# Optimization experiments

Hardware: AMD Instinct MI355X
Metric: run time of the kernel (lower is better)

## Reference

```python
import jax, jax.numpy as jnp
import numpy as np

N = 100000      # nodes
D = 64          # input feature dim
L0, L1 = 64, 32 # layer sizes
EP = 400000     # positive edges
EN = 400000     # negative edges
LAMB = 1.0


def _scatter_mean(feats, rows, num_nodes):
    # mean of feats grouped by destination node `rows`; empty nodes -> 0
    s = jax.ops.segment_sum(feats, rows, num_segments=num_nodes)
    c = jax.ops.segment_sum(jnp.ones((rows.shape[0],), feats.dtype), rows, num_segments=num_nodes)
    return s / jnp.maximum(c, 1.0)[:, None]


def _base_layer(x, edges, W, b):
    row, col = edges[0], edges[1]
    agg = _scatter_mean(x[col], row, x.shape[0])          # [N, D]
    return jnp.tanh(jnp.concatenate([agg, x], axis=1) @ W + b)


def _deep_layer(x1, x2, pos_edges, neg_edges, W, b):
    agg1 = _scatter_mean(x1[pos_edges[1]], pos_edges[0], x1.shape[0])
    agg2 = _scatter_mean(x2[neg_edges[1]], neg_edges[0], x2.shape[0])
    return jnp.tanh(jnp.concatenate([agg1, agg2, x1], axis=1) @ W + b)


def _xavier(key, shape):
    fan_in, fan_out = shape[0], shape[1]
    lim = np.sqrt(6.0 / (fan_in + fan_out)).astype(np.float32)
    return jax.random.uniform(key, shape, jnp.float32, -lim, lim)


def setup_inputs() -> dict:
    key = jax.random.key(0)
    ks = jax.random.split(key, 12)
    X = jax.random.normal(ks[0], (N, D), jnp.float32)
    W_pos0 = _xavier(ks[1], (2 * D, L0)); b_pos0 = jnp.zeros((L0,), jnp.float32)
    W_neg0 = _xavier(ks[2], (2 * D, L0)); b_neg0 = jnp.zeros((L0,), jnp.float32)
    W_pos1 = _xavier(ks[3], (3 * L0, L1)); b_pos1 = jnp.zeros((L1,), jnp.float32)
    W_neg1 = _xavier(ks[4], (3 * L0, L1)); b_neg1 = jnp.zeros((L1,), jnp.float32)
    W_reg = _xavier(ks[5], (4 * L1, 2))
    positive_edges = jax.random.randint(ks[6], (2, EP), 0, N)
    negative_edges = jax.random.randint(ks[7], (2, EN), 0, N)
    target = jax.random.randint(ks[8], (EP + EN,), 0, 2)
    pos_samples = jax.random.randint(ks[9], (EP,), 0, N)
    neg_samples = jax.random.randint(ks[10], (EN,), 0, N)
    return {"X": X, "W_pos0": W_pos0, "b_pos0": b_pos0, "W_neg0": W_neg0,
            "b_neg0": b_neg0, "W_pos1": W_pos1, "b_pos1": b_pos1,
            "W_neg1": W_neg1, "b_neg1": b_neg1, "W_reg": W_reg,
            "positive_edges": positive_edges, "negative_edges": negative_edges,
            "target": target, "pos_samples": pos_samples, "neg_samples": neg_samples}


def _triplet_loss(z, edges, samples):
    zi = z[edges[0]]
    zj = z[edges[1]]
    zk = z[samples]
    norm_ij = jnp.sum((zi - zj) ** 2, axis=1)
    norm_ik = jnp.sum((zj - zk) ** 2, axis=1)
    return jnp.mean(jnp.maximum(norm_ij - norm_ik, 0.0)), zi, zj


def reference(X, W_pos0, b_pos0, W_neg0, b_neg0, W_pos1, b_pos1,
              W_neg1, b_neg1, W_reg, positive_edges, negative_edges,
              target, pos_samples, neg_samples):
    h_pos = _base_layer(X, positive_edges, W_pos0, b_pos0)
    h_neg = _base_layer(X, negative_edges, W_neg0, b_neg0)
    h_pos2 = _deep_layer(h_pos, h_neg, positive_edges, negative_edges, W_pos1, b_pos1)
    h_neg2 = _deep_layer(h_neg, h_pos, positive_edges, negative_edges, W_neg1, b_neg1)
    z = jnp.concatenate([h_pos2, h_neg2], axis=1)  # [N, 2*L1]

    loss_pos, pzi, pzj = _triplet_loss(z, positive_edges, pos_samples)
    loss_neg, nzi, nzj = _triplet_loss(z, negative_edges, neg_samples)

    feats = jnp.concatenate([
        jnp.concatenate([pzi, pzj], axis=1),
        jnp.concatenate([nzi, nzj], axis=1)], axis=0)       # [EP+EN, 4*L1]
    logp = jax.nn.log_softmax(feats @ W_reg, axis=1)
    regress = -jnp.mean(jnp.take_along_axis(logp, target[:, None], axis=1))
    loss = regress + LAMB * (loss_pos + loss_neg)
    return (loss, z)
```

## Files before the change

kernel.cpp:

```cpp
#include <hip/hip_runtime.h>
#include <cstdint>

#define N_NODES 100000
#define EP_N 400000
#define EN_N 400000
#define NODE_BLOCKS ((N_NODES + 63) / 64)
#define DEEP_BLOCKS (N_NODES / 32)
#define SCHUNK 512
#define SBLK ((N_NODES + SCHUNK - 1) / SCHUNK)

#define BSTR 264
#define DSTR 392

#define XB_BLKS ((((N_NODES + 1) * 16) + 255) / 256)
#define WP_BLKS 112
#define CNT_BLKS (((EP_N + EN_N) + 255) / 256)
#define EI_BLKS CNT_BLKS

#define ACC_OFF 0
#define I_CNTP 16
#define I_CNTN (I_CNTP + N_NODES)
#define I_CURP (I_CNTN + N_NODES)
#define I_CURN (I_CURP + N_NODES)
#define I_OFFP (I_CURN + N_NODES)
#define I_OFFN (I_OFFP + N_NODES + 1)
#define I_CSRP (((I_OFFN + N_NODES + 1) + 3) & ~3)
#define CSR_SZ (EP_N + 4 * N_NODES)
#define I_CSRN (I_CSRP + CSR_SZ)
#define I_PART (I_CSRN + CSR_SZ)
#define I_EIDX (((I_PART + 2 * SBLK) + 3) & ~3)
#define F_XB (((I_EIDX + 4 * (EP_N + EN_N)) + 15) & ~15)
#define F_HB (F_XB + 32 * (N_NODES + 1))
#define F_HQ (F_HB + 64 * (N_NODES + 1))
#define F_PNU (F_HQ + 32 * (N_NODES + 1))
#define F_PNV (F_PNU + 4 * N_NODES)
#define F_ZQ (F_PNV + 4 * N_NODES)
#define F_WT (((F_ZQ + 16 * N_NODES) + 15) & ~15)

typedef __attribute__((ext_vector_type(8))) short sh8;
typedef __attribute__((ext_vector_type(4))) float f32x4;

__device__ inline float bf2f(unsigned short u) {
    return __uint_as_float((unsigned)u << 16);
}
__device__ inline unsigned short f2bf(float v) {
    unsigned u = __float_as_uint(v);
    return (unsigned short)((u + 0x7FFFu + ((u >> 16) & 1u)) >> 16);
}
__device__ inline float lo_bf(unsigned u) { return __uint_as_float(u << 16); }
__device__ inline float hi_bf(unsigned u) { return __uint_as_float(u & 0xFFFF0000u); }

__device__ inline float dot4f8(unsigned a, unsigned b) {
    float s = __builtin_amdgcn_cvt_f32_fp8(a, 0) * __builtin_amdgcn_cvt_f32_fp8(b, 0);
    s = fmaf(__builtin_amdgcn_cvt_f32_fp8(a, 1), __builtin_amdgcn_cvt_f32_fp8(b, 1), s);
    s = fmaf(__builtin_amdgcn_cvt_f32_fp8(a, 2), __builtin_amdgcn_cvt_f32_fp8(b, 2), s);
    s = fmaf(__builtin_amdgcn_cvt_f32_fp8(a, 3), __builtin_amdgcn_cvt_f32_fp8(b, 3), s);
    return s;
}

__global__ void prep_kernel(const float* __restrict__ X, unsigned short* __restrict__ xb,
                            const float* __restrict__ W0p, const float* __restrict__ W0n,
                            const float* __restrict__ W1p, const float* __restrict__ W1n,
                            unsigned short* __restrict__ wt,
                            const int* __restrict__ pe, const int* __restrict__ ne,
                            const int* __restrict__ ps, const int* __restrict__ ns,
                            const int* __restrict__ tgt,
                            int* cp, int* cn, int4* __restrict__ eidx) {
    int b = blockIdx.x;
    if (b < XB_BLKS) {
        int i = b * 256 + threadIdx.x;
        if (i < (N_NODES + 1) * 16) {
            ushort4 o = {0, 0, 0, 0};
            if (i < N_NODES * 16) {
                float4 v = ((const float4*)X)[i];
                o.x = f2bf(v.x); o.y = f2bf(v.y); o.z = f2bf(v.z); o.w = f2bf(v.w);
            }
            ((ushort4*)xb)[i] = o;
        }
    } else if (b < XB_BLKS + WP_BLKS) {
        int i = (b - XB_BLKS) * 256 + threadIdx.x;
        if (i < 8192) {
            int n = i >> 7, k = i & 127;
            wt[i] = f2bf(W0p[k * 64 + n]);
        } else if (i < 16384) {
            int j = i - 8192; int n = j >> 7, k = j & 127;
            wt[i] = f2bf(W0n[k * 64 + n]);
        } else if (i < 22528) {
            int j = i - 16384; int n = j / 192, k = j - n * 192;
            wt[i] = f2bf(W1p[k * 32 + n]);
        } else if (i < 28672) {
            int j = i - 22528; int n = j / 192, k = j - n * 192;
            wt[i] = f2bf(W1n[k * 32 + n]);
        }
    } else if (b < XB_BLKS + WP_BLKS + CNT_BLKS) {
        int i = (b - XB_BLKS - WP_BLKS) * 256 + threadIdx.x;
        if (i < EP_N) {
            atomicAdd(&cp[pe[i]], 1);
        } else if (i < EP_N + EN_N) {
            atomicAdd(&cn[ne[i - EP_N]], 1);
        }
    } else {
        int e = (b - XB_BLKS - WP_BLKS - CNT_BLKS) * 256 + threadIdx.x;
        if (e < EP_N) {
            int4 q = {pe[e], pe[EP_N + e], ps[e], tgt[e]};
            eidx[e] = q;
        } else if (e < EP_N + EN_N) {
            int e2 = e - EP_N;
            int4 q = {ne[e2], ne[EN_N + e2], ns[e2], tgt[e]};
            eidx[e] = q;
        }
    }
}

__global__ __launch_bounds__(512) void scan_p1(const int* __restrict__ cntP,
                                               const int* __restrict__ cntN,
                                               int* part) {
    int l = blockIdx.x < SBLK ? 0 : 1;
    int blk = blockIdx.x - l * SBLK;
    const int* cnt = l == 0 ? cntP : cntN;
    int idx = blk * SCHUNK + threadIdx.x;
    int v = idx < N_NODES ? (cnt[idx] + 3) & ~3 : 0;
    __shared__ int tmp[512];
    tmp[threadIdx.x] = v;
    __syncthreads();
    for (int d = 256; d > 0; d >>= 1) {
        if (threadIdx.x < d) tmp[threadIdx.x] += tmp[threadIdx.x + d];
        __syncthreads();
    }
    if (threadIdx.x == 0) part[l * SBLK + blk] = tmp[0];
}

__global__ __launch_bounds__(512) void scan_p2(int* part) {
    int t = threadIdx.x;
    int l = t >> 8, idx = t & 255;
    int v = idx < SBLK ? part[l * SBLK + idx] : 0;
    __shared__ int tmp[512];
    int sb = l << 8;
    tmp[sb + idx] = v;
    __syncthreads();
    for (int d = 1; d < 256; d <<= 1) {
        int x = (idx >= d) ? tmp[sb + idx - d] : 0;
        __syncthreads();
        tmp[sb + idx] += x;
        __syncthreads();
    }
    if (idx < SBLK) part[l * SBLK + idx] = tmp[sb + idx] - v;
}

__global__ __launch_bounds__(512) void scan_p3(const int* __restrict__ cntP,
                                               const int* __restrict__ cntN,
                                               const int* __restrict__ part,
                                               int* offP, int* offN,
                                               int* csrP, int* csrN) {
    int l = blockIdx.x < SBLK ? 0 : 1;
    int blk = blockIdx.x - l * SBLK;
    const int* cnt = l == 0 ? cntP : cntN;
    int* off = l == 0 ? offP : offN;
    int* csr = l == 0 ? csrP : csrN;
    int base = part[l * SBLK + blk];
    int t = threadIdx.x;
    int gidx = blk * SCHUNK + t;
    int c = gidx < N_NODES ? cnt[gidx] : 0;
    int cpad = (c + 3) & ~3;
    __shared__ int tmp[512];
    tmp[t] = cpad;
    __syncthreads();
    for (int d = 1; d < 512; d <<= 1) {
        int x = (t >= d) ? tmp[t - d] : 0;
        __syncthreads();
        tmp[t] += x;
        __syncthreads();
    }
    int incl = tmp[t];
    if (gidx < N_NODES) {
        int o = base + incl - cpad;
        off[gidx] = o;
        for (int p = c; p < cpad; ++p) csr[o + p] = N_NODES;
    }
    if (gidx == N_NODES - 1) off[N_NODES] = base + incl;
}

__global__ void fill_kernel(const int* __restrict__ pe, const int* __restrict__ ne,
                            const int* __restrict__ offP, const int* __restrict__ offN,
                            int* curP, int* curN, int* csrP, int* csrN) {
    int e = blockIdx.x * 256 + threadIdx.x;
    if (e < EP_N) {
        int row = pe[e], col = pe[EP_N + e];
        int slot = atomicAdd(&curP[row], 1);
        csrP[offP[row] + slot] = col;
    } else if (e < EP_N + EN_N) {
        int e2 = e - EP_N;
        int row = ne[e2], col = ne[EN_N + e2];
        int slot = atomicAdd(&curN[row], 1);
        csrN[offN[row] + slot] = col;
    }
}

__device__ inline void gmb2w(const unsigned* __restrict__ xb32,
                             const int* __restrict__ csrP, int pP, int enP, int cP,
                             const int* __restrict__ csrN, int pN, int enN, int cN,
                             int hf, int l5,
                             float& gP0, float& gP1, float& gN0, float& gN1) {
    float a0 = 0.f, a1 = 0.f, b0 = 0.f, b1 = 0.f;
    while (pP < enP && pN < enN) {
        int4 ca = *(const int4*)(csrP + pP);
        int4 cb = *(const int4*)(csrN + pN);
        int cA0 = hf ? ca.y : ca.x;
        int cA1 = hf ? ca.w : ca.z;
        int cB0 = hf ? cb.y : cb.x;
        int cB1 = hf ? cb.w : cb.z;
        unsigned va0 = xb32[cA0 * 32 + l5];
        unsigned va1 = xb32[cA1 * 32 + l5];
        unsigned vb0 = xb32[cB0 * 32 + l5];
        unsigned vb1 = xb32[cB1 * 32 + l5];
        a0 += lo_bf(va0) + lo_bf(va1);
        a1 += hi_bf(va0) + hi_bf(va1);
        b0 += lo_bf(vb0) + lo_bf(vb1);
        b1 += hi_bf(vb0) + hi_bf(vb1);
        pP += 4; pN += 4;
    }
    for (; pP < enP; pP += 4) {
        int4 ca = *(const int4*)(csrP + pP);
        int cA0 = hf ? ca.y : ca.x;
        int cA1 = hf ? ca.w : ca.z;
        unsigned va0 = xb32[cA0 * 32 + l5];
        unsigned va1 = xb32[cA1 * 32 + l5];
        a0 += lo_bf(va0) + lo_bf(va1);
        a1 += hi_bf(va0) + hi_bf(va1);
    }
    for (; pN < enN; pN += 4) {
        int4 cb = *(const int4*)(csrN + pN);
        int cB0 = hf ? cb.y : cb.x;
        int cB1 = hf ? cb.w : cb.z;
        unsigned vb0 = xb32[cB0 * 32 + l5];
        unsigned vb1 = xb32[cB1 * 32 + l5];
        b0 += lo_bf(vb0) + lo_bf(vb1);
        b1 += hi_bf(vb0) + hi_bf(vb1);
    }
    a0 += __shfl_xor(a0, 32); a1 += __shfl_xor(a1, 32);
    b0 += __shfl_xor(b0, 32); b1 += __shfl_xor(b1, 32);
    float rP = 1.f / fmaxf((float)cP, 1.f), rN = 1.f / fmaxf((float)cN, 1.f);
    gP0 = a0 * rP; gP1 = a1 * rP;
    gN0 = b0 * rN; gN1 = b1 * rN;
}

__device__ inline void gd2q(const unsigned* __restrict__ hq32,
                            const int* __restrict__ csrP, int pP, int enP, int cP,
                            const int* __restrict__ csrN, int pN, int enN, int cN,
                            int hf, int l5,
                            float& gPp0, float& gPp1, float& gPn0, float& gPn1,
                            float& gNp0, float& gNp1, float& gNn0, float& gNn1) {
    float ap0 = 0.f, ap1 = 0.f, an0 = 0.f, an1 = 0.f;
    float bp0 = 0.f, bp1 = 0.f, bn0 = 0.f, bn1 = 0.f;
    while (pP < enP && pN < enN) {
        int4 ca = *(const int4*)(csrP + pP);
        int4 cb = *(const int4*)(csrN + pN);
        int cA0 = hf ? ca.y : ca.x;
        int cA1 = hf ? ca.w : ca.z;
        int cB0 = hf ? cb.y : cb.x;
        int cB1 = hf ? cb.w : cb.z;
        unsigned va0 = hq32[cA0 * 32 + l5];
        unsigned va1 = hq32[cA1 * 32 + l5];
        unsigned vb0 = hq32[cB0 * 32 + l5];
        unsigned vb1 = hq32[cB1 * 32 + l5];
        ap0 += __builtin_amdgcn_cvt_f32_fp8(va0, 0) + __builtin_amdgcn_cvt_f32_fp8(va1, 0);
        an0 += __builtin_amdgcn_cvt_f32_fp8(va0, 1) + __builtin_amdgcn_cvt_f32_fp8(va1, 1);
        ap1 += __builtin_amdgcn_cvt_f32_fp8(va0, 2) + __builtin_amdgcn_cvt_f32_fp8(va1, 2);
        an1 += __builtin_amdgcn_cvt_f32_fp8(va0, 3) + __builtin_amdgcn_cvt_f32_fp8(va1, 3);
        bp0 += __builtin_amdgcn_cvt_f32_fp8(vb0, 0) + __builtin_amdgcn_cvt_f32_fp8(vb1, 0);
        bn0 += __builtin_amdgcn_cvt_f32_fp8(vb0, 1) + __builtin_amdgcn_cvt_f32_fp8(vb1, 1);
        bp1 += __builtin_amdgcn_cvt_f32_fp8(vb0, 2) + __builtin_amdgcn_cvt_f32_fp8(vb1, 2);
        bn1 += __builtin_amdgcn_cvt_f32_fp8(vb0, 3) + __builtin_amdgcn_cvt_f32_fp8(vb1, 3);
        pP += 4; pN += 4;
    }
    for (; pP < enP; pP += 4) {
        int4 ca = *(const int4*)(csrP + pP);
        int cA0 = hf ? ca.y : ca.x;
        int cA1 = hf ? ca.w : ca.z;
        unsigned va0 = hq32[cA0 * 32 + l5];
        unsigned va1 = hq32[cA1 * 32 + l5];
        ap0 += __builtin_amdgcn_cvt_f32_fp8(va0, 0) + __builtin_amdgcn_cvt_f32_fp8(va1, 0);
        an0 += __builtin_amdgcn_cvt_f32_fp8(va0, 1) + __builtin_amdgcn_cvt_f32_fp8(va1, 1);
        ap1 += __builtin_amdgcn_cvt_f32_fp8(va0, 2) + __builtin_amdgcn_cvt_f32_fp8(va1, 2);
        an1 += __builtin_amdgcn_cvt_f32_fp8(va0, 3) + __builtin_amdgcn_cvt_f32_fp8(va1, 3);
    }
    for (; pN < enN; pN += 4) {
        int4 cb = *(const int4*)(csrN + pN);
        int cB0 = hf ? cb.y : cb.x;
        int cB1 = hf ? cb.w : cb.z;
        unsigned vb0 = hq32[cB0 * 32 + l5];
        unsigned vb1 = hq32[cB1 * 32 + l5];
        bp0 += __builtin_amdgcn_cvt_f32_fp8(vb0, 0) + __builtin_amdgcn_cvt_f32_fp8(vb1, 0);
        bn0 += __builtin_amdgcn_cvt_f32_fp8(vb0, 1) + __builtin_amdgcn_cvt_f32_fp8(vb1, 1);
        bp1 += __builtin_amdgcn_cvt_f32_fp8(vb0, 2) + __builtin_amdgcn_cvt_f32_fp8(vb1, 2);
        bn1 += __builtin_amdgcn_cvt_f32_fp8(vb0, 3) + __builtin_amdgcn_cvt_f32_fp8(vb1, 3);
    }
    ap0 += __shfl_xor(ap0, 32); ap1 += __shfl_xor(ap1, 32);
    an0 += __shfl_xor(an0, 32); an1 += __shfl_xor(an1, 32);
    bp0 += __shfl_xor(bp0, 32); bp1 += __shfl_xor(bp1, 32);
    bn0 += __shfl_xor(bn0, 32); bn1 += __shfl_xor(bn1, 32);
    float rP = 1.f / fmaxf((float)cP, 1.f), rN = 1.f / fmaxf((float)cN, 1.f);
    gPp0 = ap0 * rP; gPp1 = ap1 * rP; gPn0 = an0 * rP; gPn1 = an1 * rP;
    gNp0 = bp0 * rN; gNp1 = bp1 * rN; gNn0 = bn0 * rN; gNn1 = bn1 * rN;
}

__global__ __launch_bounds__(512) void base_both(
    const unsigned short* __restrict__ xb,
    const int* __restrict__ offP, const int* __restrict__ csrP,
    const int* __restrict__ offN, const int* __restrict__ csrN,
    const int* __restrict__ cntP, const int* __restrict__ cntN,
    const unsigned short* __restrict__ wt0,
    const float* __restrict__ bp0, const float* __restrict__ bn0,
    unsigned short* __restrict__ hboth, unsigned* __restrict__ hq32) {
    __shared__ unsigned short lds[64 * BSTR];
    int tid = threadIdx.x, lane = tid & 63, w = tid >> 6;
    int hf = lane >> 5, l5 = lane & 31;
    int base = blockIdx.x * 64;
    const unsigned* xb32 = (const unsigned*)xb;
    if (blockIdx.x == 0 && tid < 64) ((unsigned*)hboth)[N_NODES * 64 + tid] = 0u;
    if (blockIdx.x == 0 && tid < 32) hq32[N_NODES * 32 + tid] = 0u;
    for (int r = w * 8; r < w * 8 + 8; ++r) {
        int node = base + r;
        float gP0 = 0.f, gP1 = 0.f, gN0 = 0.f, gN1 = 0.f;
        unsigned sxv = 0;
        if (node < N_NODES) {
            gmb2w(xb32, csrP, offP[node], offP[node + 1], cntP[node],
                  csrN, offN[node], offN[node + 1], cntN[node], hf, l5,
                  gP0, gP1, gN0, gN1);
            sxv = xb32[node * 32 + l5];
        }
        unsigned* rp32 = (unsigned*)&lds[r * BSTR];
        if (hf == 0) {
            rp32[l5] = (unsigned)f2bf(gP0) | ((unsigned)f2bf(gP1) << 16);
            rp32[32 + l5] = sxv;
        } else {
            rp32[64 + l5] = (unsigned)f2bf(gN0) | ((unsigned)f2bf(gN1) << 16);
            rp32[96 + l5] = sxv;
        }
    }
    __syncthreads();
    int wu = __builtin_amdgcn_readfirstlane(w);
    int mt = wu >> 1, half = wu & 1;
    int l15 = lane & 15, kq = lane >> 4;
    const unsigned short* wbase = wt0 + half * 8192;
    f32x4 acc[4];
#pragma unroll
    for (int nt = 0; nt < 4; ++nt) acc[nt] = (f32x4){0.f, 0.f, 0.f, 0.f};
    const unsigned short* arow = &lds[(mt * 16 + l15) * BSTR + half * 128 + kq * 8];
#pragma unroll
    for (int ks = 0; ks < 4; ++ks) {
        sh8 a = *(const sh8*)(arow + ks * 32);
#pragma unroll
        for (int nt = 0; nt < 4; ++nt) {
            sh8 bf = *(const sh8*)(wbase + (nt * 16 + l15) * 128 + ks * 32 + kq * 8);
            acc[nt] = __builtin_amdgcn_mfma_f32_16x16x32_bf16(a, bf, acc[nt], 0, 0, 0);
        }
    }
    __syncthreads();
    float* ht = (float*)lds;
    const float* bias = half ? bn0 : bp0;
#pragma unroll
    for (int nt = 0; nt < 4; ++nt) {
        int col = nt * 16 + l15;
        float bb = bias[col];
#pragma unroll
        for (int r = 0; r < 4; ++r) {
            int row = mt * 16 + kq * 4 + r;
            ht[row * 130 + half * 64 + col] = tanhf(acc[nt][r] + bb);
        }
    }
    __syncthreads();
    unsigned* hb32 = (unsigned*)hboth;
    for (int i = tid; i < 64 * 64; i += 512) {
        int rr = i >> 6, c = i & 63;
        int node = base + rr;
        if (node < N_NODES) {
            unsigned lo = f2bf(ht[rr * 130 + c]);
            unsigned hi = f2bf(ht[rr * 130 + 64 + c]);
            hb32[node * 64 + c] = lo | (hi << 16);
        }
    }
    for (int i = tid; i < 64 * 32; i += 512) {
        int rr = i >> 5, c2 = i & 31;
        int node = base + rr;
        if (node < N_NODES) {
            float hp0 = ht[rr * 130 + 2 * c2];
            float hn0 = ht[rr * 130 + 64 + 2 * c2];
            float hp1 = ht[rr * 130 + 2 * c2 + 1];
            float hn1 = ht[rr * 130 + 64 + 2 * c2 + 1];
            int lo = __builtin_amdgcn_cvt_pk_fp8_f32(hp0, hn0, 0, false);
            int q = __builtin_amdgcn_cvt_pk_fp8_f32(hp1, hn1, lo, true);
            hq32[node * 32 + c2] = (unsigned)q;
        }
    }
}

__global__ __launch_bounds__(512) void deep_both(
    const unsigned short* __restrict__ hb, const unsigned* __restrict__ hq32,
    const int* __restrict__ offP, const int* __restrict__ csrP,
    const int* __restrict__ offN, const int* __restrict__ csrN,
    const int* __restrict__ cntP, const int* __restrict__ cntN,
    const unsigned short* __restrict__ wt1,
    const float* __restrict__ bp1, const float* __restrict__ bn1,
    const float* __restrict__ Wreg, float* __restrict__ z,
    unsigned char* __restrict__ zq, float4* __restrict__ pnu,
    float4* __restrict__ pnv) {
    __shared__ unsigned short lds[32 * DSTR];
    int tid = threadIdx.x, lane = tid & 63, w = tid >> 6;
    int hf = lane >> 5, l5 = lane & 31;
    int base = blockIdx.x * 32;
    const unsigned* hb32 = (const unsigned*)hb;
    for (int r = w * 4; r < w * 4 + 4; ++r) {
        int node = base + r;
        float gPp0, gPp1, gPn0, gPn1, gNp0, gNp1, gNn0, gNn1;
        gd2q(hq32, csrP, offP[node], offP[node + 1], cntP[node],
             csrN, offN[node], offN[node + 1], cntN[node], hf, l5,
             gPp0, gPp1, gPn0, gPn1, gNp0, gNp1, gNn0, gNn1);
        uint2 sv = *(const uint2*)(hb32 + node * 64 + l5 * 2);
        unsigned* rp32 = (unsigned*)&lds[r * DSTR];
        if (hf == 0) {
            rp32[l5] = (unsigned)f2bf(gPp0) | ((unsigned)f2bf(gPp1) << 16);
            rp32[32 + l5] = (unsigned)f2bf(gNn0) | ((unsigned)f2bf(gNn1) << 16);
            rp32[64 + l5] = (sv.x & 0xFFFFu) | ((sv.y & 0xFFFFu) << 16);
        } else {
            rp32[96 + l5] = (unsigned)f2bf(gPn0) | ((unsigned)f2bf(gPn1) << 16);
            rp32[128 + l5] = (unsigned)f2bf(gNp0) | ((unsigned)f2bf(gNp1) << 16);
            rp32[160 + l5] = (sv.x >> 16) | (sv.y & 0xFFFF0000u);
        }
    }
    __syncthreads();
    int wu = __builtin_amdgcn_readfirstlane(w);
    int mt = wu >> 2, half = (wu >> 1) & 1, nt = wu & 1;
    int l15 = lane & 15, kq = lane >> 4;
    const unsigned short* wbase = wt1 + half * 6144;
    f32x4 acc = (f32x4){0.f, 0.f, 0.f, 0.f};
    const unsigned short* arow = &lds[(mt * 16 + l15) * DSTR + half * 192 + kq * 8];
#pragma unroll
    for (int ks = 0; ks < 6; ++ks) {
        sh8 a = *(const sh8*)(arow + ks * 32);
        sh8 bf = *(const sh8*)(wbase + (nt * 16 + l15) * 192 + ks * 32 + kq * 8);
        acc = __builtin_amdgcn_mfma_f32_16x16x32_bf16(a, bf, acc, 0, 0, 0);
    }
    __syncthreads();
    float* ot = (float*)lds;
    {
        const float* bias = half ? bn1 : bp1;
        int col = nt * 16 + l15;
        float bb = bias[col];
#pragma unroll
        for (int r = 0; r < 4; ++r) {
            int row = mt * 16 + kq * 4 + r;
            ot[row * 65 + half * 32 + col] = tanhf(acc[r] + bb);
        }
    }
    __syncthreads();
    for (int r = w * 4; r < w * 4 + 4; ++r) {
        int node = base + r;
        float v = ot[r * 65 + lane];
        z[node * 64 + lane] = v;
        int pq = __builtin_amdgcn_cvt_pk_fp8_f32(v, v, 0, false);
        zq[node * 64 + lane] = (unsigned char)(pq & 0xFF);
        float vq = __builtin_amdgcn_cvt_f32_fp8(pq, 0);
        float u0 = vq * Wreg[lane * 2 + 0];
        float u1 = vq * Wreg[lane * 2 + 1];
        float v0 = vq * Wreg[128 + lane * 2 + 0];
        float v1 = vq * Wreg[128 + lane * 2 + 1];
        float s = vq * vq;
#pragma unroll
        for (int off = 32; off; off >>= 1) {
            u0 += __shfl_xor(u0, off);
            u1 += __shfl_xor(u1, off);
            v0 += __shfl_xor(v0, off);
            v1 += __shfl_xor(v1, off);
            s += __shfl_xor(s, off);
        }
        if (lane == 0) {
            float4 su = {u0, u1, s, 0.f};
            float4 sv2 = {v0, v1, s, 0.f};
            pnu[node] = su;
            pnv[node] = sv2;
        }
    }
}

__global__ __launch_bounds__(256) void loss6_kernel(
    const unsigned char* __restrict__ zq, const float4* __restrict__ pnu,
    const float4* __restrict__ pnv, const int4* __restrict__ eidx, float* acc) {
    int tid = threadIdx.x;
    int lane = tid & 63;
    int g = lane >> 2, sub = lane & 3;
    int wid = (blockIdx.x * 256 + tid) >> 6;
    int nw = (gridDim.x * 256) >> 6;
    float s_p = 0.f, s_n = 0.f, s_r = 0.f;
    const float q = 0.25f;
    for (int eb = wid * 32; eb < EP_N + EN_N; eb += nw * 32) {
        int eA = eb + g, eB = eb + 16 + g;
        bool vA = eA < EP_N + EN_N, vB = eB < EP_N + EN_N;
        bool pA = eA < EP_N, pB = eB < EP_N;
        int4 qA = eidx[vA ? eA : 0];
        int4 qB = eidx[vB ? eB : 0];
        uint4 ziA = *(const uint4*)(zq + ((long long)qA.x << 6) + (sub << 4));
        uint4 zjA = *(const uint4*)(zq + ((long long)qA.y << 6) + (sub << 4));
        uint4 zkA = *(const uint4*)(zq + ((long long)qA.z << 6) + (sub << 4));
        uint4 ziB = *(const uint4*)(zq + ((long long)qB.x << 6) + (sub << 4));
        uint4 zjB = *(const uint4*)(zq + ((long long)qB.y << 6) + (sub << 4));
        uint4 zkB = *(const uint4*)(zq + ((long long)qB.z << 6) + (sub << 4));
        float4 uA = pnu[qA.x];
        float4 wA = pnv[qA.y];
        float skA = pnu[qA.z].z;
        float4 uB = pnu[qB.x];
        float4 wB = pnv[qB.y];
        float skB = pnu[qB.z].z;
        float d1A = dot4f8(ziA.x, zjA.x) + dot4f8(ziA.y, zjA.y) +
                    dot4f8(ziA.z, zjA.z) + dot4f8(ziA.w, zjA.w);
        float d2A = dot4f8(zjA.x, zkA.x) + dot4f8(zjA.y, zkA.y) +
                    dot4f8(zjA.z, zkA.z) + dot4f8(zjA.w, zkA.w);
        float d1B = dot4f8(ziB.x, zjB.x) + dot4f8(ziB.y, zjB.y) +
                    dot4f8(ziB.z, zjB.z) + dot4f8(ziB.w, zjB.w);
        float d2B = dot4f8(zjB.x, zkB.x) + dot4f8(zjB.y, zkB.y) +
                    dot4f8(zjB.z, zkB.z) + dot4f8(zjB.w, zkB.w);
#pragma unroll
        for (int off = 1; off < 4; off <<= 1) {
            d1A += __shfl_xor(d1A, off);
            d2A += __shfl_xor(d2A, off);
            d1B += __shfl_xor(d1B, off);
            d2B += __shfl_xor(d2B, off);
        }
        if (vA) {
            float nij = uA.z + wA.z - 2.f * d1A;
            float nik = wA.z + skA - 2.f * d2A;
            float tri = fmaxf(nij - nik, 0.f);
            float l0 = uA.x + wA.x, l1 = uA.y + wA.y;
            float m = fmaxf(l0, l1);
            float lse = m + logf(expf(l0 - m) + expf(l1 - m));
            s_r += (lse - (qA.w ? l1 : l0)) * q;
            if (pA) s_p += tri * q; else s_n += tri * q;
        }
        if (vB) {
            float nij = uB.z + wB.z - 2.f * d1B;
            float nik = wB.z + skB - 2.f * d2B;
            float tri = fmaxf(nij - nik, 0.f);
            float l0 = uB.x + wB.x, l1 = uB.y + wB.y;
            float m = fmaxf(l0, l1);
            float lse = m + logf(expf(l0 - m) + expf(l1 - m));
            s_r += (lse - (qB.w ? l1 : l0)) * q;
            if (pB) s_p += tri * q; else s_n += tri * q;
        }
    }
#pragma unroll
    for (int off = 32; off; off >>= 1) {
        s_p += __shfl_xor(s_p, off);
        s_n += __shfl_xor(s_n, off);
        s_r += __shfl_xor(s_r, off);
    }
    __shared__ float red[3][4];
    int w = tid >> 6;
    if (lane == 0) {
        red[0][w] = s_p; red[1][w] = s_n; red[2][w] = s_r;
    }
    __syncthreads();
    if (tid == 0) {
        atomicAdd(&acc[0], red[0][0] + red[0][1] + red[0][2] + red[0][3]);
        atomicAdd(&acc[1], red[1][0] + red[1][1] + red[1][2] + red[1][3]);
        atomicAdd(&acc[2], red[2][0] + red[2][1] + red[2][2] + red[2][3]);
    }
}

__global__ void finalize_kernel(const float* __restrict__ acc, float* out) {
    out[0] = acc[2] / (float)(EP_N + EN_N) +
             1.0f * (acc[0] / (float)EP_N + acc[1] / (float)EN_N);
}

extern "C" void kernel_launch(void* const* d_in, const int* in_sizes, int n_in,
                              void* d_out, int out_size, void* d_ws, size_t ws_size,
                              hipStream_t stream) {
    const float* X = (const float*)d_in[0];
    const float* W_pos0 = (const float*)d_in[1];
    const float* b_pos0 = (const float*)d_in[2];
    const float* W_neg0 = (const float*)d_in[3];
    const float* b_neg0 = (const float*)d_in[4];
    const float* W_pos1 = (const float*)d_in[5];
    const float* b_pos1 = (const float*)d_in[6];
    const float* W_neg1 = (const float*)d_in[7];
    const float* b_neg1 = (const float*)d_in[8];
    const float* W_reg = (const float*)d_in[9];
    const int* pe = (const int*)d_in[10];
    const int* ne = (const int*)d_in[11];
    const int* target = (const int*)d_in[12];
    const int* ps = (const int*)d_in[13];
    const int* ns = (const int*)d_in[14];
    float* out = (float*)d_out;
    float* ws = (float*)d_ws;
    int* wsi = (int*)d_ws;

    float* acc = ws + ACC_OFF;
    int* cntP = wsi + I_CNTP;
    int* cntN = wsi + I_CNTN;
    int* curP = wsi + I_CURP;
    int* curN = wsi + I_CURN;
    int* offP = wsi + I_OFFP;
    int* offN = wsi + I_OFFN;
    int* csrP = wsi + I_CSRP;
    int* csrN = wsi + I_CSRN;
    int* part = wsi + I_PART;
    int4* eidx = (int4*)(wsi + I_EIDX);
    unsigned short* xb = (unsigned short*)(ws + F_XB);
    unsigned short* hboth = (unsigned short*)(ws + F_HB);
    unsigned* hq32 = (unsigned*)(ws + F_HQ);
    float4* pnu = (float4*)(ws + F_PNU);
    float4* pnv = (float4*)(ws + F_PNV);
    unsigned char* zq = (unsigned char*)(ws + F_ZQ);
    unsigned short* wt = (unsigned short*)(ws + F_WT);
    float* z = out + 1;

    hipMemsetAsync(ws, 0, (size_t)(16 + 4 * N_NODES) * sizeof(float), stream);

    prep_kernel<<<XB_BLKS + WP_BLKS + CNT_BLKS + EI_BLKS, 256, 0, stream>>>(
        X, xb, W_pos0, W_neg0, W_pos1, W_neg1, wt, pe, ne, ps, ns, target,
        cntP, cntN, eidx);
    scan_p1<<<2 * SBLK, 512, 0, stream>>>(cntP, cntN, part);
    scan_p2<<<1, 512, 0, stream>>>(part);
    scan_p3<<<2 * SBLK, 512, 0, stream>>>(cntP, cntN, part, offP, offN, csrP, csrN);
    fill_kernel<<<(EP_N + EN_N + 255) / 256, 256, 0, stream>>>(pe, ne, offP, offN,
                                                               curP, curN, csrP, csrN);

    base_both<<<NODE_BLOCKS, 512, 0, stream>>>(xb, offP, csrP, offN, csrN, cntP, cntN,
                                               wt, b_pos0, b_neg0, hboth, hq32);
    deep_both<<<DEEP_BLOCKS, 512, 0, stream>>>(hboth, hq32, offP, csrP, offN, csrN,
                                               cntP, cntN, wt + 16384, b_pos1, b_neg1,
                                               W_reg, z, zq, pnu, pnv);

    loss6_kernel<<<2048, 256, 0, stream>>>(zq, pnu, pnv, eidx, acc);
    finalize_kernel<<<1, 1, 0, stream>>>(acc, out);
}
```

Measured before the change: 350.4 us.

## Write loss edge records in CSR row-sorted order during fill

Computes unpadded per-row offsets alongside the padded CSR offsets in the scan kernels, and has fill_kernel scatter each edge's (row, col, sample, target) record into row-sorted position instead of prep_kernel copying them in input order. This gives the loss kernel better locality when gathering per-node data for row endpoints, and removes a separate pass over the edge arrays. In exchange, the record writes become scattered and the scans do extra work.

Measured after the change: 347.9 us. About the same (-0.7%).

```diff
diff --git a/kernel.cpp b/kernel.cpp
--- a/kernel.cpp
+++ b/kernel.cpp
@@ -15,7 +15,6 @@
 #define XB_BLKS ((((N_NODES + 1) * 16) + 255) / 256)
 #define WP_BLKS 112
 #define CNT_BLKS (((EP_N + EN_N) + 255) / 256)
-#define EI_BLKS CNT_BLKS
 
 #define ACC_OFF 0
 #define I_CNTP 16
@@ -24,11 +23,13 @@
 #define I_CURN (I_CURP + N_NODES)
 #define I_OFFP (I_CURN + N_NODES)
 #define I_OFFN (I_OFFP + N_NODES + 1)
-#define I_CSRP (((I_OFFN + N_NODES + 1) + 3) & ~3)
+#define I_OFFPC (I_OFFN + N_NODES + 1)
+#define I_OFFNC (I_OFFPC + N_NODES + 1)
+#define I_CSRP (((I_OFFNC + N_NODES + 1) + 3) & ~3)
 #define CSR_SZ (EP_N + 4 * N_NODES)
 #define I_CSRN (I_CSRP + CSR_SZ)
 #define I_PART (I_CSRN + CSR_SZ)
-#define I_EIDX (((I_PART + 2 * SBLK) + 3) & ~3)
+#define I_EIDX (((I_PART + 4 * SBLK) + 3) & ~3)
 #define F_XB (((I_EIDX + 4 * (EP_N + EN_N)) + 15) & ~15)
 #define F_HB (F_XB + 32 * (N_NODES + 1))
 #define F_HQ (F_HB + 64 * (N_NODES + 1))
@@ -63,9 +64,7 @@
                             const float* __restrict__ W1p, const float* __restrict__ W1n,
                             unsigned short* __restrict__ wt,
                             const int* __restrict__ pe, const int* __restrict__ ne,
-                            const int* __restrict__ ps, const int* __restrict__ ns,
-                            const int* __restrict__ tgt,
-                            int* cp, int* cn, int4* __restrict__ eidx) {
+                            int* cp, int* cn) {
     int b = blockIdx.x;
     if (b < XB_BLKS) {
         int i = b * 256 + threadIdx.x;
@@ -92,22 +91,12 @@
             int j = i - 22528; int n = j / 192, k = j - n * 192;
             wt[i] = f2bf(W1n[k * 32 + n]);
         }
-    } else if (b < XB_BLKS + WP_BLKS + CNT_BLKS) {
+    } else {
         int i = (b - XB_BLKS - WP_BLKS) * 256 + threadIdx.x;
         if (i < EP_N) {
             atomicAdd(&cp[pe[i]], 1);
         } else if (i < EP_N + EN_N) {
             atomicAdd(&cn[ne[i - EP_N]], 1);
-        }
-    } else {
-        int e = (b - XB_BLKS - WP_BLKS - CNT_BLKS) * 256 + threadIdx.x;
-        if (e < EP_N) {
-            int4 q = {pe[e], pe[EP_N + e], ps[e], tgt[e]};
-            eidx[e] = q;
-        } else if (e < EP_N + EN_N) {
-            int e2 = e - EP_N;
-            int4 q = {ne[e2], ne[EN_N + e2], ns[e2], tgt[e]};
-            eidx[e] = q;
         }
     }
 }
@@ -119,22 +108,31 @@
     int blk = blockIdx.x - l * SBLK;
     const int* cnt = l == 0 ? cntP : cntN;
     int idx = blk * SCHUNK + threadIdx.x;
-    int v = idx < N_NODES ? (cnt[idx] + 3) & ~3 : 0;
+    int c = idx < N_NODES ? cnt[idx] : 0;
+    int vp = (c + 3) & ~3;
     __shared__ int tmp[512];
-    tmp[threadIdx.x] = v;
+    __shared__ int tmp2[512];
+    tmp[threadIdx.x] = vp;
+    tmp2[threadIdx.x] = c;
     __syncthreads();
     for (int d = 256; d > 0; d >>= 1) {
-        if (threadIdx.x < d) tmp[threadIdx.x] += tmp[threadIdx.x + d];
+        if (threadIdx.x < d) {
+            tmp[threadIdx.x] += tmp[threadIdx.x + d];
+            tmp2[threadIdx.x] += tmp2[threadIdx.x + d];
+        }
         __syncthreads();
     }
-    if (threadIdx.x == 0) part[l * SBLK + blk] = tmp[0];
-}
-
-__global__ __launch_bounds__(512) void scan_p2(int* part) {
+    if (threadIdx.x == 0) {
+        part[l * SBLK + blk] = tmp[0];
+        part[(2 + l) * SBLK + blk] = tmp2[0];
+    }
+}
+
+__global__ __launch_bounds__(1024) void scan_p2(int* part) {
     int t = threadIdx.x;
     int l = t >> 8, idx = t & 255;
     int v = idx < SBLK ? part[l * SBLK + idx] : 0;
-    __shared__ int tmp[512];
+    __shared__ int tmp[1024];
     int sb = l << 8;
     tmp[sb + idx] = v;
     __syncthreads();
@@ -151,48 +149,67 @@
                                                const int* __restrict__ cntN,
                                                const int* __restrict__ part,
                                                int* offP, int* offN,
+                                               int* offPc, int* offNc,
                                                int* csrP, int* csrN) {
     int l = blockIdx.x < SBLK ? 0 : 1;
     int blk = blockIdx.x - l * SBLK;
     const int* cnt = l == 0 ? cntP : cntN;
     int* off = l == 0 ? offP : offN;
+    int* offc = l == 0 ? offPc : offNc;
     int* csr = l == 0 ? csrP : csrN;
     int base = part[l * SBLK + blk];
+    int basec = part[(2 + l) * SBLK + blk];
     int t = threadIdx.x;
     int gidx = blk * SCHUNK + t;
     int c = gidx < N_NODES ? cnt[gidx] : 0;
     int cpad = (c + 3) & ~3;
     __shared__ int tmp[512];
+    __shared__ int tmp2[512];
     tmp[t] = cpad;
+    tmp2[t] = c;
     __syncthreads();
     for (int d = 1; d < 512; d <<= 1) {
         int x = (t >= d) ? tmp[t - d] : 0;
+        int x2 = (t >= d) ? tmp2[t - d] : 0;
         __syncthreads();
         tmp[t] += x;
+        tmp2[t] += x2;
         __syncthreads();
     }
-    int incl = tmp[t];
+    int incl = tmp[t], inclc = tmp2[t];
     if (gidx < N_NODES) {
         int o = base + incl - cpad;
         off[gidx] = o;
+        offc[gidx] = basec + inclc - c;
         for (int p = c; p < cpad; ++p) csr[o + p] = N_NODES;
     }
-    if (gidx == N_NODES - 1) off[N_NODES] = base + incl;
+    if (gidx == N_NODES - 1) {
+        off[N_NODES] = base + incl;
+        offc[N_NODES] = basec + inclc;
+    }
 }
 
 __global__ void fill_kernel(const int* __restrict__ pe, const int* __restrict__ ne,
                             const int* __restrict__ offP, const int* __restrict__ offN,
-                            int* curP, int* curN, int* csrP, int* csrN) {
+                            const int* __restrict__ offPc, const int* __restrict__ offNc,
+                            const int* __restrict__ ps, const int* __restrict__ ns,
+                            const int* __restrict__ tgt,
+                            int* curP, int* curN, int* csrP, int* csrN,
+                            int4* __restrict__ eidx) {
     int e = blockIdx.x * 256 + threadIdx.x;
     if (e < EP_N) {
         int row = pe[e], col = pe[EP_N + e];
         int slot = atomicAdd(&curP[row], 1);
         csrP[offP[row] + slot] = col;
+        int4 q = {row, col, ps[e], tgt[e]};
+        eidx[offPc[row] + slot] = q;
     } else if (e < EP_N + EN_N) {
         int e2 = e - EP_N;
         int row = ne[e2], col = ne[EN_N + e2];
         int slot = atomicAdd(&curN[row], 1);
         csrN[offN[row] + slot] = col;
+        int4 q = {row, col, ns[e2], tgt[e]};
+        eidx[EP_N + offNc[row] + slot] = q;
     }
 }
 
@@ -600,6 +617,8 @@
     int* curN = wsi + I_CURN;
     int* offP = wsi + I_OFFP;
     int* offN = wsi + I_OFFN;
+    int* offPc = wsi + I_OFFPC;
+    int* offNc = wsi + I_OFFNC;
     int* csrP = wsi + I_CSRP;
     int* csrN = wsi + I_CSRN;
     int* part = wsi + I_PART;
@@ -615,14 +634,15 @@
 
     hipMemsetAsync(ws, 0, (size_t)(16 + 4 * N_NODES) * sizeof(float), stream);
 
-    prep_kernel<<<XB_BLKS + WP_BLKS + CNT_BLKS + EI_BLKS, 256, 0, stream>>>(
-        X, xb, W_pos0, W_neg0, W_pos1, W_neg1, wt, pe, ne, ps, ns, target,
-        cntP, cntN, eidx);
+    prep_kernel<<<XB_BLKS + WP_BLKS + CNT_BLKS, 256, 0, stream>>>(
+        X, xb, W_pos0, W_neg0, W_pos1, W_neg1, wt, pe, ne, cntP, cntN);
     scan_p1<<<2 * SBLK, 512, 0, stream>>>(cntP, cntN, part);
-    scan_p2<<<1, 512, 0, stream>>>(part);
-    scan_p3<<<2 * SBLK, 512, 0, stream>>>(cntP, cntN, part, offP, offN, csrP, csrN);
-    fill_kernel<<<(EP_N + EN_N + 255) / 256, 256, 0, stream>>>(pe, ne, offP, offN,
-                                                               curP, curN, csrP, csrN);
+    scan_p2<<<1, 1024, 0, stream>>>(part);
+    scan_p3<<<2 * SBLK, 512, 0, stream>>>(cntP, cntN, part, offP, offN,
+                                          offPc, offNc, csrP, csrN);
+    fill_kernel<<<(EP_N + EN_N + 255) / 256, 256, 0, stream>>>(
+        pe, ne, offP, offN, offPc, offNc, ps, ns, target,
+        curP, curN, csrP, csrN, eidx);
 
     base_both<<<NODE_BLOCKS, 512, 0, stream>>>(xb, offP, csrP, offN, csrN, cntP, cntN,
                                                wt, b_pos0, b_neg0, hboth, hq32);
```
